# Optimization experiments

Hardware: AMD Instinct MI355X
Metric: run time of the kernel (lower is better)

## Reference

```python
import jax, jax.numpy as jnp
import numpy as np


def setup_inputs() -> dict:
    key = jax.random.key(0)
    ks = jax.random.split(key, 7)
    B, L, D, H = 256, 1024, 768, 768
    x = jax.random.normal(ks[0], (B, L, D), dtype=jnp.float32)
    label_mask = jax.random.randint(ks[1], (B, L), 0, 2).astype(jnp.int32)
    global_prototype_tensor = jax.random.normal(ks[2], (L + 1, D), dtype=jnp.float32)
    W_h = jax.random.normal(ks[3], (H, D), dtype=jnp.float32) * 0.02
    b_h = jax.random.normal(ks[4], (H,), dtype=jnp.float32) * 0.02
    W_p = jax.random.normal(ks[5], (D, H), dtype=jnp.float32) * 0.02
    b_p = jax.random.normal(ks[6], (D,), dtype=jnp.float32) * 0.02
    return {"x": x, "label_mask": label_mask,
            "global_prototype_tensor": global_prototype_tensor,
            "W_h": W_h, "b_h": b_h, "W_p": W_p, "b_p": b_p}


def _mlp(v, W_h, b_h, W_p, b_p):
    # torch Linear: y = v @ W.T + b
    h = jax.nn.relu(jnp.einsum('ld,hd->lh', v, W_h) + b_h)
    return jnp.einsum('lh,dh->ld', h, W_p) + b_p


def reference(x, label_mask, global_prototype_tensor, W_h, b_h, W_p, b_p):
    # x: [B, L, D]; label_mask: [B, L] (1 if label i in example's label_list)
    m = label_mask.astype(x.dtype)                        # [B, L]
    pos_cnt = m.sum(0)                                    # [L]
    B = x.shape[0]
    anti_cnt = B - pos_cnt                                # [L]
    pos_sum = jnp.einsum('bl,bld->ld', m, x)              # masked segment-sum
    tot_sum = x.sum(0)                                    # [L, D]
    anti_sum = tot_sum - pos_sum

    pos_mean = pos_sum / jnp.maximum(pos_cnt, 1.0)[:, None]
    anti_mean = anti_sum / jnp.maximum(anti_cnt, 1.0)[:, None]

    avg_pos = 0.5 * pos_mean + 0.5 * global_prototype_tensor[:-1]   # [L, D]
    avg_anti = 0.5 * anti_mean + 0.5 * global_prototype_tensor[-1]  # [L, D]

    proto = _mlp(avg_pos, W_h, b_h, W_p, b_p)
    proto = jnp.where((pos_cnt > 0)[:, None], proto, 0.0)           # rows stay zero if no members

    anti_proto = _mlp(avg_anti, W_h, b_h, W_p, b_p)
    w = (anti_cnt > 0).astype(x.dtype)                              # [L]
    anti = jnp.einsum('l,ld->d', w, anti_proto) / jnp.maximum(w.sum(), 1.0)

    return jnp.concatenate([proto, anti[None, :]], axis=0)          # [L+1, D]
```

## Files before the change

### kernel.cpp

```cpp
#include <hip/hip_runtime.h>

#define L_DIM 1024
#define B_DIM 256
#define D_DIM 768
#define K_DIM 768
#define NT    (K_DIM / 32)
#define WN    (768 * 768)

typedef _Float16 half8 __attribute__((ext_vector_type(8)));
typedef float    floatx4 __attribute__((ext_vector_type(4)));

__device__ __forceinline__ ushort f2h(float f) {
    _Float16 h = (_Float16)f;
    return __builtin_bit_cast(ushort, h);
}
__device__ __forceinline__ float h2f(ushort u) {
    return (float)__builtin_bit_cast(_Float16, u);
}

__device__ __forceinline__ void gl16(const ushort* g, ushort* l) {
    __builtin_amdgcn_global_load_lds(
        (const __attribute__((address_space(1))) unsigned int*)g,
        (__attribute__((address_space(3))) unsigned int*)l, 16, 0, 0);
}

__global__ __launch_bounds__(768)
void reduce_and_cast(const float* __restrict__ x,
                     const int* __restrict__ mask,
                     const float* __restrict__ gpt,
                     const float* __restrict__ Wh, const float* __restrict__ Wp,
                     ushort* __restrict__ Vhi, ushort* __restrict__ Vlo,
                     ushort* __restrict__ WhH, ushort* __restrict__ WpH,
                     float* __restrict__ pos_cnt)
{
    const int tid = threadIdx.x;

    if (blockIdx.x >= 256) {
        const int idx = ((blockIdx.x - 256) * 768 + tid) * 4;
        const float4 v = (idx < WN) ? *(const float4*)(Wh + idx)
                                    : *(const float4*)(Wp + (idx - WN));
        ushort4 o;
        o.x = f2h(v.x); o.y = f2h(v.y); o.z = f2h(v.z); o.w = f2h(v.w);
        if (idx < WN) *(ushort4*)(WhH + idx) = o;
        else          *(ushort4*)(WpH + (idx - WN)) = o;
        return;
    }

    __shared__ int mS[256][4];
    const int l0 = blockIdx.x * 4;
    if (tid < 256)
        *(int4*)&mS[tid][0] = *(const int4*)(mask + (size_t)tid * L_DIM + l0);
    __syncthreads();

    const int row = tid / 192;
    const int t   = tid % 192;
    const int d0  = t * 4;
    const int l   = l0 + row;

    const size_t bstride = (size_t)L_DIM * D_DIM;
    const float* xp = x + (size_t)l * D_DIM + d0;

    floatx4 pos = {0.f, 0.f, 0.f, 0.f};
    floatx4 tot = {0.f, 0.f, 0.f, 0.f};
    float cnt = 0.f;

    #pragma unroll 16
    for (int b = 0; b < B_DIM; ++b) {
        const floatx4 v = __builtin_nontemporal_load((const floatx4*)(xp + (size_t)b * bstride));
        const float fm = (float)mS[b][row];
        tot += v;
        pos[0] = fmaf(fm, v[0], pos[0]);
        pos[1] = fmaf(fm, v[1], pos[1]);
        pos[2] = fmaf(fm, v[2], pos[2]);
        pos[3] = fmaf(fm, v[3], pos[3]);
        cnt += fm;
    }

    const float inv_p = 0.5f / fmaxf(cnt, 1.0f);
    const float inv_a = 0.5f / fmaxf((float)B_DIM - cnt, 1.0f);

    const float4 g4  = *(const float4*)(gpt + (size_t)l * D_DIM + d0);
    const float4 gl4 = *(const float4*)(gpt + (size_t)L_DIM * D_DIM + d0);

    float vp[4], va[4];
    vp[0] = pos[0] * inv_p + 0.5f * g4.x;
    vp[1] = pos[1] * inv_p + 0.5f * g4.y;
    vp[2] = pos[2] * inv_p + 0.5f * g4.z;
    vp[3] = pos[3] * inv_p + 0.5f * g4.w;
    va[0] = (tot[0] - pos[0]) * inv_a + 0.5f * gl4.x;
    va[1] = (tot[1] - pos[1]) * inv_a + 0.5f * gl4.y;
    va[2] = (tot[2] - pos[2]) * inv_a + 0.5f * gl4.z;
    va[3] = (tot[3] - pos[3]) * inv_a + 0.5f * gl4.w;

    ushort4 ph, pl, ah, al;
    ph.x = f2h(vp[0]); pl.x = f2h(vp[0] - h2f(ph.x));
    ph.y = f2h(vp[1]); pl.y = f2h(vp[1] - h2f(ph.y));
    ph.z = f2h(vp[2]); pl.z = f2h(vp[2] - h2f(ph.z));
    ph.w = f2h(vp[3]); pl.w = f2h(vp[3] - h2f(ph.w));
    ah.x = f2h(va[0]); al.x = f2h(va[0] - h2f(ah.x));
    ah.y = f2h(va[1]); al.y = f2h(va[1] - h2f(ah.y));
    ah.z = f2h(va[2]); al.z = f2h(va[2] - h2f(ah.z));
    ah.w = f2h(va[3]); al.w = f2h(va[3] - h2f(ah.w));

    const size_t r0 = (size_t)l * D_DIM + d0;
    const size_t r1 = (size_t)(L_DIM + l) * D_DIM + d0;
    *(ushort4*)(Vhi + r0) = ph;  *(ushort4*)(Vlo + r0) = pl;
    *(ushort4*)(Vhi + r1) = ah;  *(ushort4*)(Vlo + r1) = al;

    if (t == 0) pos_cnt[l] = cnt;
}

template<int MODE>
__global__ __launch_bounds__(256)
void gemm_split(const ushort* __restrict__ Ahi, const ushort* __restrict__ Alo,
                const ushort* __restrict__ Bh, const float* __restrict__ bias,
                ushort* __restrict__ OutHi, ushort* __restrict__ OutLo,
                float* __restrict__ OutF, float* __restrict__ Partial,
                const float* __restrict__ cnt)
{
    __shared__ ushort lds[2][3][64 * 32];
    __shared__ float  colsum[4][32];

    const int tid  = threadIdx.x;
    const int lane = tid & 63;
    const int wid  = tid >> 6;
    const int brow = blockIdx.y * 64;
    const int bcol = blockIdx.x * 64;
    const int wr   = (wid >> 1) * 32;
    const int wc   = (wid & 1) * 32;

    const int srow = tid >> 2;
    const int slot = tid & 3;
    const int sk   = (slot ^ ((srow >> 1) & 3)) * 8;

    const ushort* pAh = Ahi + (size_t)(brow + srow) * K_DIM + sk;
    const ushort* pAl = Alo + (size_t)(brow + srow) * K_DIM + sk;
    const ushort* pBh = Bh  + (size_t)(bcol + srow) * K_DIM + sk;

    const int ldst = tid * 8;

    const int q   = lane >> 4;
    const int rA  = wr + (lane & 15);
    const int rB  = wc + (lane & 15);
    const int fA  = rA * 32 + ((q ^ ((rA >> 1) & 3)) << 3);
    const int fB  = rB * 32 + ((q ^ ((rB >> 1) & 3)) << 3);

    floatx4 acc[2][2] = {};

    gl16(pAh, &lds[0][0][ldst]);
    gl16(pAl, &lds[0][1][ldst]);
    gl16(pBh, &lds[0][2][ldst]);
    __syncthreads();

    for (int t = 0; t < NT; ++t) {
        const int cur = t & 1;
        if (t + 1 < NT) {
            const int ko = (t + 1) * 32;
            const int nxt = cur ^ 1;
            gl16(pAh + ko, &lds[nxt][0][ldst]);
            gl16(pAl + ko, &lds[nxt][1][ldst]);
            gl16(pBh + ko, &lds[nxt][2][ldst]);
        }
        half8 ah0 = *(half8*)&lds[cur][0][fA];
        half8 ah1 = *(half8*)&lds[cur][0][fA + 512];
        half8 al0 = *(half8*)&lds[cur][1][fA];
        half8 al1 = *(half8*)&lds[cur][1][fA + 512];
        half8 bh0 = *(half8*)&lds[cur][2][fB];
        half8 bh1 = *(half8*)&lds[cur][2][fB + 512];

        acc[0][0] = __builtin_amdgcn_mfma_f32_16x16x32_f16(ah0, bh0, acc[0][0], 0, 0, 0);
        acc[0][1] = __builtin_amdgcn_mfma_f32_16x16x32_f16(ah0, bh1, acc[0][1], 0, 0, 0);
        acc[1][0] = __builtin_amdgcn_mfma_f32_16x16x32_f16(ah1, bh0, acc[1][0], 0, 0, 0);
        acc[1][1] = __builtin_amdgcn_mfma_f32_16x16x32_f16(ah1, bh1, acc[1][1], 0, 0, 0);
        acc[0][0] = __builtin_amdgcn_mfma_f32_16x16x32_f16(al0, bh0, acc[0][0], 0, 0, 0);
        acc[0][1] = __builtin_amdgcn_mfma_f32_16x16x32_f16(al0, bh1, acc[0][1], 0, 0, 0);
        acc[1][0] = __builtin_amdgcn_mfma_f32_16x16x32_f16(al1, bh0, acc[1][0], 0, 0, 0);
        acc[1][1] = __builtin_amdgcn_mfma_f32_16x16x32_f16(al1, bh1, acc[1][1], 0, 0, 0);

        __syncthreads();
    }

    if (MODE == 0 || brow < L_DIM) {
        #pragma unroll
        for (int mi = 0; mi < 2; ++mi) {
            #pragma unroll
            for (int ni = 0; ni < 2; ++ni) {
                const int col   = bcol + wc + ni * 16 + (lane & 15);
                const int rbase = brow + wr + mi * 16 + ((lane >> 4) << 2);
                const float bv = bias[col];
                #pragma unroll
                for (int r = 0; r < 4; ++r) {
                    const float v = acc[mi][ni][r] + bv;
                    const int row = rbase + r;
                    if (MODE == 0) {
                        const float h = fmaxf(v, 0.f);
                        const ushort hh = f2h(h);
                        OutHi[(size_t)row * D_DIM + col] = hh;
                        OutLo[(size_t)row * D_DIM + col] = f2h(h - h2f(hh));
                    } else {
                        OutF[(size_t)row * D_DIM + col] = (cnt[row] > 0.f) ? v : 0.f;
                    }
                }
            }
        }
    } else {
        float s[2] = {0.f, 0.f};
        #pragma unroll
        for (int mi = 0; mi < 2; ++mi) {
            const int rbase = brow + wr + mi * 16 + ((lane >> 4) << 2);
            #pragma unroll
            for (int r = 0; r < 4; ++r) {
                const float w = (cnt[rbase + r - L_DIM] < 255.5f) ? 1.0f : 0.0f;
                #pragma unroll
                for (int ni = 0; ni < 2; ++ni) {
                    const int col = bcol + wc + ni * 16 + (lane & 15);
                    s[ni] = fmaf(w, acc[mi][ni][r] + bias[col], s[ni]);
                }
            }
        }
        #pragma unroll
        for (int ni = 0; ni < 2; ++ni) {
            s[ni] += __shfl_down(s[ni], 32);
            s[ni] += __shfl_down(s[ni], 16);
            if (lane < 16) colsum[wid][ni * 16 + lane] = s[ni];
        }
        __syncthreads();
        if (tid < 64) {
            const float v = (tid < 32)
                ? colsum[0][tid] + colsum[2][tid]
                : colsum[1][tid - 32] + colsum[3][tid - 32];
            Partial[(size_t)(blockIdx.y - 16) * D_DIM + bcol + tid] = v;
        }
    }
}

__global__ __launch_bounds__(256)
void finalize_anti(const float* __restrict__ Partial,
                   const float* __restrict__ cnt,
                   float* __restrict__ out)
{
    const int d = blockIdx.x * 256 + threadIdx.x;
    float s = 0.f;
    #pragma unroll
    for (int p = 0; p < 16; ++p) s += Partial[(size_t)p * D_DIM + d];
    float wsum = 0.f;
    #pragma unroll 8
    for (int l = 0; l < L_DIM; ++l) wsum += (cnt[l] < 255.5f) ? 1.0f : 0.0f;
    out[(size_t)L_DIM * D_DIM + d] = s / fmaxf(wsum, 1.0f);
}

extern "C" void kernel_launch(void* const* d_in, const int* in_sizes, int n_in,
                              void* d_out, int out_size, void* d_ws, size_t ws_size,
                              hipStream_t stream) {
    const float* x    = (const float*)d_in[0];
    const int*   mask = (const int*)d_in[1];
    const float* gpt  = (const float*)d_in[2];
    const float* W_h  = (const float*)d_in[3];
    const float* b_h  = (const float*)d_in[4];
    const float* W_p  = (const float*)d_in[5];
    const float* b_p  = (const float*)d_in[6];
    float* out = (float*)d_out;

    char* p = (char*)d_ws;
    ushort* Vhi  = (ushort*)p; p += (size_t)2 * L_DIM * D_DIM * 2;
    ushort* Vlo  = (ushort*)p; p += (size_t)2 * L_DIM * D_DIM * 2;
    ushort* Hhi  = (ushort*)p; p += (size_t)2 * L_DIM * D_DIM * 2;
    ushort* Hlo  = (ushort*)p; p += (size_t)2 * L_DIM * D_DIM * 2;
    ushort* WhH  = (ushort*)p; p += (size_t)WN * 2;
    ushort* WpH  = (ushort*)p; p += (size_t)WN * 2;
    float*  Part = (float*)p;  p += (size_t)16 * D_DIM * 4;
    float*  cnt  = (float*)p;

    reduce_and_cast<<<640, 768, 0, stream>>>(x, mask, gpt, W_h, W_p,
                                             Vhi, Vlo, WhH, WpH, cnt);

    dim3 ggrid(D_DIM / 64, 2 * L_DIM / 64);
    gemm_split<0><<<ggrid, 256, 0, stream>>>(Vhi, Vlo, WhH, b_h,
                                             Hhi, Hlo, nullptr, nullptr, nullptr);
    gemm_split<1><<<ggrid, 256, 0, stream>>>(Hhi, Hlo, WpH, b_p,
                                             nullptr, nullptr, out, Part, cnt);

    finalize_anti<<<3, 256, 0, stream>>>(Part, cnt, out);
}
```

Measured before the change: 187.0 us.

## Split batch reduction across two block halves with a separate combine kernel

The reduction over the batch now runs in twice as many smaller blocks: each block covers two labels and half of the batch, and writes partial pos/tot sums and counts to workspace. A new combine kernel adds the two partials, applies the mean and prototype blend, and emits the hi/lo half-precision split. The weight-cast blocks are reorganised to 384 threads and placed first in the grid. The aim is more parallelism and better occupancy on the bandwidth-bound read of x, at the cost of an extra kernel launch and a write and read of the partial buffers.

```diff
diff --git a/kernel.cpp b/kernel.cpp
--- a/kernel.cpp
+++ b/kernel.cpp
@@ -6,6 +6,8 @@
 #define K_DIM 768
 #define NT    (K_DIM / 32)
 #define WN    (768 * 768)
+#define CAST_BLOCKS 768
+#define RED_BLOCKS  1024
 
 typedef _Float16 half8 __attribute__((ext_vector_type(8)));
 typedef float    floatx4 __attribute__((ext_vector_type(4)));
@@ -24,19 +26,18 @@
         (__attribute__((address_space(3))) unsigned int*)l, 16, 0, 0);
 }
 
-__global__ __launch_bounds__(768)
+__global__ __launch_bounds__(384, 6)
 void reduce_and_cast(const float* __restrict__ x,
                      const int* __restrict__ mask,
-                     const float* __restrict__ gpt,
                      const float* __restrict__ Wh, const float* __restrict__ Wp,
-                     ushort* __restrict__ Vhi, ushort* __restrict__ Vlo,
-                     ushort* __restrict__ WhH, ushort* __restrict__ WpH,
-                     float* __restrict__ pos_cnt)
+                     float* __restrict__ posP, float* __restrict__ totP,
+                     float* __restrict__ cntP,
+                     ushort* __restrict__ WhH, ushort* __restrict__ WpH)
 {
     const int tid = threadIdx.x;
 
-    if (blockIdx.x >= 256) {
-        const int idx = ((blockIdx.x - 256) * 768 + tid) * 4;
+    if (blockIdx.x < CAST_BLOCKS) {
+        const int idx = (blockIdx.x * 384 + tid) * 4;
         const float4 v = (idx < WN) ? *(const float4*)(Wh + idx)
                                     : *(const float4*)(Wp + (idx - WN));
         ushort4 o;
@@ -46,10 +47,14 @@
         return;
     }
 
-    __shared__ int mS[256][4];
-    const int l0 = blockIdx.x * 4;
-    if (tid < 256)
-        *(int4*)&mS[tid][0] = *(const int4*)(mask + (size_t)tid * L_DIM + l0);
+    const int bi = blockIdx.x - CAST_BLOCKS;
+    const int lq = bi >> 1;
+    const int bh = bi & 1;
+    const int l0 = lq * 2;
+
+    __shared__ int mS[128][2];
+    if (tid < 128)
+        *(int2*)&mS[tid][0] = *(const int2*)(mask + (size_t)(bh * 128 + tid) * L_DIM + l0);
     __syncthreads();
 
     const int row = tid / 192;
@@ -58,14 +63,14 @@
     const int l   = l0 + row;
 
     const size_t bstride = (size_t)L_DIM * D_DIM;
-    const float* xp = x + (size_t)l * D_DIM + d0;
+    const float* xp = x + (size_t)(bh * 128) * bstride + (size_t)l * D_DIM + d0;
 
     floatx4 pos = {0.f, 0.f, 0.f, 0.f};
     floatx4 tot = {0.f, 0.f, 0.f, 0.f};
     float cnt = 0.f;
 
-    #pragma unroll 16
-    for (int b = 0; b < B_DIM; ++b) {
+    #pragma unroll 8
+    for (int b = 0; b < 128; ++b) {
         const floatx4 v = __builtin_nontemporal_load((const floatx4*)(xp + (size_t)b * bstride));
         const float fm = (float)mS[b][row];
         tot += v;
@@ -76,6 +81,32 @@
         cnt += fm;
     }
 
+    const size_t po = (size_t)(bh * L_DIM + l) * D_DIM + d0;
+    *(floatx4*)(posP + po) = pos;
+    *(floatx4*)(totP + po) = tot;
+    if (t == 0) cntP[bh * L_DIM + l] = cnt;
+}
+
+__global__ __launch_bounds__(192)
+void combine_build_v(const float* __restrict__ posP, const float* __restrict__ totP,
+                     const float* __restrict__ cntP,
+                     const float* __restrict__ gpt,
+                     ushort* __restrict__ Vhi, ushort* __restrict__ Vlo,
+                     float* __restrict__ pos_cnt)
+{
+    const int l  = blockIdx.x;
+    const int d0 = threadIdx.x * 4;
+    const size_t o0 = (size_t)l * D_DIM + d0;
+    const size_t o1 = (size_t)(L_DIM + l) * D_DIM + d0;
+
+    const floatx4 p0 = *(const floatx4*)(posP + o0);
+    const floatx4 p1 = *(const floatx4*)(posP + o1);
+    const floatx4 t0 = *(const floatx4*)(totP + o0);
+    const floatx4 t1 = *(const floatx4*)(totP + o1);
+    const floatx4 pos = p0 + p1;
+    const floatx4 tot = t0 + t1;
+    const float cnt = cntP[l] + cntP[L_DIM + l];
+
     const float inv_p = 0.5f / fmaxf(cnt, 1.0f);
     const float inv_a = 0.5f / fmaxf((float)B_DIM - cnt, 1.0f);
 
@@ -102,12 +133,10 @@
     ah.z = f2h(va[2]); al.z = f2h(va[2] - h2f(ah.z));
     ah.w = f2h(va[3]); al.w = f2h(va[3] - h2f(ah.w));
 
-    const size_t r0 = (size_t)l * D_DIM + d0;
-    const size_t r1 = (size_t)(L_DIM + l) * D_DIM + d0;
-    *(ushort4*)(Vhi + r0) = ph;  *(ushort4*)(Vlo + r0) = pl;
-    *(ushort4*)(Vhi + r1) = ah;  *(ushort4*)(Vlo + r1) = al;
-
-    if (t == 0) pos_cnt[l] = cnt;
+    *(ushort4*)(Vhi + o0) = ph;  *(ushort4*)(Vlo + o0) = pl;
+    *(ushort4*)(Vhi + o1) = ah;  *(ushort4*)(Vlo + o1) = al;
+
+    if (threadIdx.x == 0) pos_cnt[l] = cnt;
 }
 
 template<int MODE>
@@ -268,11 +297,16 @@
     ushort* Hlo  = (ushort*)p; p += (size_t)2 * L_DIM * D_DIM * 2;
     ushort* WhH  = (ushort*)p; p += (size_t)WN * 2;
     ushort* WpH  = (ushort*)p; p += (size_t)WN * 2;
+    float*  posP = (float*)p;  p += (size_t)2 * L_DIM * D_DIM * 4;
+    float*  totP = (float*)p;  p += (size_t)2 * L_DIM * D_DIM * 4;
+    float*  cntP = (float*)p;  p += (size_t)2 * L_DIM * 4;
     float*  Part = (float*)p;  p += (size_t)16 * D_DIM * 4;
     float*  cnt  = (float*)p;
 
-    reduce_and_cast<<<640, 768, 0, stream>>>(x, mask, gpt, W_h, W_p,
-                                             Vhi, Vlo, WhH, WpH, cnt);
+    reduce_and_cast<<<CAST_BLOCKS + RED_BLOCKS, 384, 0, stream>>>(
+        x, mask, W_h, W_p, posP, totP, cntP, WhH, WpH);
+
+    combine_build_v<<<L_DIM, 192, 0, stream>>>(posP, totP, cntP, gpt, Vhi, Vlo, cnt);
 
     dim3 ggrid(D_DIM / 64, 2 * L_DIM / 64);
     gemm_split<0><<<ggrid, 256, 0, stream>>>(Vhi, Vlo, WhH, b_h,
```

Measured after the change: 214.5 us. +14.7%, slower.

## Widen GEMM tiles to 64x128 and fold anti-finalize into last block

Applied to the files above, without the earlier changes.

The split-precision GEMM tile grows from 64x64 to 64x128 columns per block, so each wave computes 2x4 MFMA tiles and A-fragment loads are reused across more columns. The grid shrinks from 384 to 192 blocks. The separate finalize_anti launch is removed: the last block of the second GEMM, found with an atomic counter and threadfence, sums the partials and weights. This saves a launch and reduces A traffic, at the cost of fewer blocks (192 on a 256-CU part), which leaves compute units idle, plus a serial tail in the last block.

```diff
diff --git a/kernel.cpp b/kernel.cpp
--- a/kernel.cpp
+++ b/kernel.cpp
@@ -4,7 +4,7 @@
 #define B_DIM 256
 #define D_DIM 768
 #define K_DIM 768
-#define NT    (K_DIM / 32)
+#define NTILES (K_DIM / 32)
 #define WN    (768 * 768)
 
 typedef _Float16 half8 __attribute__((ext_vector_type(8)));
@@ -31,7 +31,7 @@
                      const float* __restrict__ Wh, const float* __restrict__ Wp,
                      ushort* __restrict__ Vhi, ushort* __restrict__ Vlo,
                      ushort* __restrict__ WhH, ushort* __restrict__ WpH,
-                     float* __restrict__ pos_cnt)
+                     float* __restrict__ pos_cnt, unsigned* __restrict__ counter)
 {
     const int tid = threadIdx.x;
 
@@ -45,6 +45,8 @@
         else          *(ushort4*)(WpH + (idx - WN)) = o;
         return;
     }
+
+    if (blockIdx.x == 0 && tid == 0) *counter = 0u;
 
     __shared__ int mS[256][4];
     const int l0 = blockIdx.x * 4;
@@ -116,18 +118,20 @@
                 const ushort* __restrict__ Bh, const float* __restrict__ bias,
                 ushort* __restrict__ OutHi, ushort* __restrict__ OutLo,
                 float* __restrict__ OutF, float* __restrict__ Partial,
-                const float* __restrict__ cnt)
+                const float* __restrict__ cnt, unsigned* __restrict__ counter)
 {
-    __shared__ ushort lds[2][3][64 * 32];
-    __shared__ float  colsum[4][32];
+    __shared__ ushort lds[2][8192];
+    __shared__ float  colsum[4][64];
+    __shared__ float  red[256];
+    __shared__ unsigned lastflag;
 
     const int tid  = threadIdx.x;
     const int lane = tid & 63;
     const int wid  = tid >> 6;
     const int brow = blockIdx.y * 64;
-    const int bcol = blockIdx.x * 64;
+    const int bcol = blockIdx.x * 128;
     const int wr   = (wid >> 1) * 32;
-    const int wc   = (wid & 1) * 32;
+    const int wc   = (wid & 1) * 64;
 
     const int srow = tid >> 2;
     const int slot = tid & 3;
@@ -135,47 +139,60 @@
 
     const ushort* pAh = Ahi + (size_t)(brow + srow) * K_DIM + sk;
     const ushort* pAl = Alo + (size_t)(brow + srow) * K_DIM + sk;
-    const ushort* pBh = Bh  + (size_t)(bcol + srow) * K_DIM + sk;
+    const ushort* pB0 = Bh  + (size_t)(bcol + srow) * K_DIM + sk;
+    const ushort* pB1 = Bh  + (size_t)(bcol + 64 + srow) * K_DIM + sk;
 
     const int ldst = tid * 8;
 
-    const int q   = lane >> 4;
-    const int rA  = wr + (lane & 15);
-    const int rB  = wc + (lane & 15);
-    const int fA  = rA * 32 + ((q ^ ((rA >> 1) & 3)) << 3);
-    const int fB  = rB * 32 + ((q ^ ((rB >> 1) & 3)) << 3);
-
-    floatx4 acc[2][2] = {};
-
-    gl16(pAh, &lds[0][0][ldst]);
-    gl16(pAl, &lds[0][1][ldst]);
-    gl16(pBh, &lds[0][2][ldst]);
+    const int q  = lane >> 4;
+    const int rA = wr + (lane & 15);
+    const int rB = wc + (lane & 15);
+    const int fA = rA * 32 + ((q ^ ((rA >> 1) & 3)) << 3);
+    const int fB = 4096 + rB * 32 + ((q ^ ((rB >> 1) & 3)) << 3);
+
+    floatx4 acc[2][4] = {};
+
+    gl16(pAh, &lds[0][ldst]);
+    gl16(pAl, &lds[0][2048 + ldst]);
+    gl16(pB0, &lds[0][4096 + ldst]);
+    gl16(pB1, &lds[0][6144 + ldst]);
     __syncthreads();
 
-    for (int t = 0; t < NT; ++t) {
+    for (int t = 0; t < NTILES; ++t) {
         const int cur = t & 1;
-        if (t + 1 < NT) {
+        if (t + 1 < NTILES) {
             const int ko = (t + 1) * 32;
             const int nxt = cur ^ 1;
-            gl16(pAh + ko, &lds[nxt][0][ldst]);
-            gl16(pAl + ko, &lds[nxt][1][ldst]);
-            gl16(pBh + ko, &lds[nxt][2][ldst]);
-        }
-        half8 ah0 = *(half8*)&lds[cur][0][fA];
-        half8 ah1 = *(half8*)&lds[cur][0][fA + 512];
-        half8 al0 = *(half8*)&lds[cur][1][fA];
-        half8 al1 = *(half8*)&lds[cur][1][fA + 512];
-        half8 bh0 = *(half8*)&lds[cur][2][fB];
-        half8 bh1 = *(half8*)&lds[cur][2][fB + 512];
-
-        acc[0][0] = __builtin_amdgcn_mfma_f32_16x16x32_f16(ah0, bh0, acc[0][0], 0, 0, 0);
-        acc[0][1] = __builtin_amdgcn_mfma_f32_16x16x32_f16(ah0, bh1, acc[0][1], 0, 0, 0);
-        acc[1][0] = __builtin_amdgcn_mfma_f32_16x16x32_f16(ah1, bh0, acc[1][0], 0, 0, 0);
-        acc[1][1] = __builtin_amdgcn_mfma_f32_16x16x32_f16(ah1, bh1, acc[1][1], 0, 0, 0);
-        acc[0][0] = __builtin_amdgcn_mfma_f32_16x16x32_f16(al0, bh0, acc[0][0], 0, 0, 0);
-        acc[0][1] = __builtin_amdgcn_mfma_f32_16x16x32_f16(al0, bh1, acc[0][1], 0, 0, 0);
-        acc[1][0] = __builtin_amdgcn_mfma_f32_16x16x32_f16(al1, bh0, acc[1][0], 0, 0, 0);
-        acc[1][1] = __builtin_amdgcn_mfma_f32_16x16x32_f16(al1, bh1, acc[1][1], 0, 0, 0);
+            gl16(pAh + ko, &lds[nxt][ldst]);
+            gl16(pAl + ko, &lds[nxt][2048 + ldst]);
+            gl16(pB0 + ko, &lds[nxt][4096 + ldst]);
+            gl16(pB1 + ko, &lds[nxt][6144 + ldst]);
+        }
+        half8 ah0 = *(half8*)&lds[cur][fA];
+        half8 ah1 = *(half8*)&lds[cur][fA + 512];
+        half8 al0 = *(half8*)&lds[cur][2048 + fA];
+        half8 al1 = *(half8*)&lds[cur][2048 + fA + 512];
+        half8 b0  = *(half8*)&lds[cur][fB];
+        half8 b1  = *(half8*)&lds[cur][fB + 512];
+        half8 b2  = *(half8*)&lds[cur][fB + 1024];
+        half8 b3  = *(half8*)&lds[cur][fB + 1536];
+
+        acc[0][0] = __builtin_amdgcn_mfma_f32_16x16x32_f16(ah0, b0, acc[0][0], 0, 0, 0);
+        acc[0][1] = __builtin_amdgcn_mfma_f32_16x16x32_f16(ah0, b1, acc[0][1], 0, 0, 0);
+        acc[0][2] = __builtin_amdgcn_mfma_f32_16x16x32_f16(ah0, b2, acc[0][2], 0, 0, 0);
+        acc[0][3] = __builtin_amdgcn_mfma_f32_16x16x32_f16(ah0, b3, acc[0][3], 0, 0, 0);
+        acc[1][0] = __builtin_amdgcn_mfma_f32_16x16x32_f16(ah1, b0, acc[1][0], 0, 0, 0);
+        acc[1][1] = __builtin_amdgcn_mfma_f32_16x16x32_f16(ah1, b1, acc[1][1], 0, 0, 0);
+        acc[1][2] = __builtin_amdgcn_mfma_f32_16x16x32_f16(ah1, b2, acc[1][2], 0, 0, 0);
+        acc[1][3] = __builtin_amdgcn_mfma_f32_16x16x32_f16(ah1, b3, acc[1][3], 0, 0, 0);
+        acc[0][0] = __builtin_amdgcn_mfma_f32_16x16x32_f16(al0, b0, acc[0][0], 0, 0, 0);
+        acc[0][1] = __builtin_amdgcn_mfma_f32_16x16x32_f16(al0, b1, acc[0][1], 0, 0, 0);
+        acc[0][2] = __builtin_amdgcn_mfma_f32_16x16x32_f16(al0, b2, acc[0][2], 0, 0, 0);
+        acc[0][3] = __builtin_amdgcn_mfma_f32_16x16x32_f16(al0, b3, acc[0][3], 0, 0, 0);
+        acc[1][0] = __builtin_amdgcn_mfma_f32_16x16x32_f16(al1, b0, acc[1][0], 0, 0, 0);
+        acc[1][1] = __builtin_amdgcn_mfma_f32_16x16x32_f16(al1, b1, acc[1][1], 0, 0, 0);
+        acc[1][2] = __builtin_amdgcn_mfma_f32_16x16x32_f16(al1, b2, acc[1][2], 0, 0, 0);
+        acc[1][3] = __builtin_amdgcn_mfma_f32_16x16x32_f16(al1, b3, acc[1][3], 0, 0, 0);
 
         __syncthreads();
     }
@@ -184,9 +201,9 @@
         #pragma unroll
         for (int mi = 0; mi < 2; ++mi) {
             #pragma unroll
-            for (int ni = 0; ni < 2; ++ni) {
+            for (int ni = 0; ni < 4; ++ni) {
                 const int col   = bcol + wc + ni * 16 + (lane & 15);
-                const int rbase = brow + wr + mi * 16 + ((lane >> 4) << 2);
+                const int rbase = brow + wr + mi * 16 + (q << 2);
                 const float bv = bias[col];
                 #pragma unroll
                 for (int r = 0; r < 4; ++r) {
@@ -204,49 +221,60 @@
             }
         }
     } else {
-        float s[2] = {0.f, 0.f};
+        float s[4] = {0.f, 0.f, 0.f, 0.f};
         #pragma unroll
         for (int mi = 0; mi < 2; ++mi) {
-            const int rbase = brow + wr + mi * 16 + ((lane >> 4) << 2);
+            const int rbase = brow + wr + mi * 16 + (q << 2);
             #pragma unroll
             for (int r = 0; r < 4; ++r) {
                 const float w = (cnt[rbase + r - L_DIM] < 255.5f) ? 1.0f : 0.0f;
                 #pragma unroll
-                for (int ni = 0; ni < 2; ++ni) {
+                for (int ni = 0; ni < 4; ++ni) {
                     const int col = bcol + wc + ni * 16 + (lane & 15);
                     s[ni] = fmaf(w, acc[mi][ni][r] + bias[col], s[ni]);
                 }
             }
         }
         #pragma unroll
-        for (int ni = 0; ni < 2; ++ni) {
+        for (int ni = 0; ni < 4; ++ni) {
             s[ni] += __shfl_down(s[ni], 32);
             s[ni] += __shfl_down(s[ni], 16);
             if (lane < 16) colsum[wid][ni * 16 + lane] = s[ni];
         }
         __syncthreads();
-        if (tid < 64) {
-            const float v = (tid < 32)
+        if (tid < 128) {
+            const float v = (tid < 64)
                 ? colsum[0][tid] + colsum[2][tid]
-                : colsum[1][tid - 32] + colsum[3][tid - 32];
+                : colsum[1][tid - 64] + colsum[3][tid - 64];
             Partial[(size_t)(blockIdx.y - 16) * D_DIM + bcol + tid] = v;
         }
+        __threadfence();
+        __syncthreads();
+        if (tid == 0) lastflag = (atomicAdd(counter, 1u) == 95u) ? 1u : 0u;
+        __syncthreads();
+        if (lastflag) {
+            __threadfence();
+            float w = 0.f;
+            for (int i = tid; i < L_DIM; i += 256)
+                w += (cnt[i] < 255.5f) ? 1.0f : 0.0f;
+            red[tid] = w;
+            __syncthreads();
+            for (int st = 128; st > 0; st >>= 1) {
+                if (tid < st) red[tid] += red[tid + st];
+                __syncthreads();
+            }
+            const float wsum = fmaxf(red[0], 1.0f);
+            #pragma unroll
+            for (int j = 0; j < 3; ++j) {
+                const int d = tid + j * 256;
+                float sm = 0.f;
+                #pragma unroll
+                for (int pp = 0; pp < 16; ++pp)
+                    sm += Partial[(size_t)pp * D_DIM + d];
+                OutF[(size_t)L_DIM * D_DIM + d] = sm / wsum;
+            }
+        }
     }
-}
-
-__global__ __launch_bounds__(256)
-void finalize_anti(const float* __restrict__ Partial,
-                   const float* __restrict__ cnt,
-                   float* __restrict__ out)
-{
-    const int d = blockIdx.x * 256 + threadIdx.x;
-    float s = 0.f;
-    #pragma unroll
-    for (int p = 0; p < 16; ++p) s += Partial[(size_t)p * D_DIM + d];
-    float wsum = 0.f;
-    #pragma unroll 8
-    for (int l = 0; l < L_DIM; ++l) wsum += (cnt[l] < 255.5f) ? 1.0f : 0.0f;
-    out[(size_t)L_DIM * D_DIM + d] = s / fmaxf(wsum, 1.0f);
 }
 
 extern "C" void kernel_launch(void* const* d_in, const int* in_sizes, int n_in,
@@ -269,16 +297,15 @@
     ushort* WhH  = (ushort*)p; p += (size_t)WN * 2;
     ushort* WpH  = (ushort*)p; p += (size_t)WN * 2;
     float*  Part = (float*)p;  p += (size_t)16 * D_DIM * 4;
-    float*  cnt  = (float*)p;
+    float*  cnt  = (float*)p;  p += (size_t)L_DIM * 4;
+    unsigned* counter = (unsigned*)p;
 
     reduce_and_cast<<<640, 768, 0, stream>>>(x, mask, gpt, W_h, W_p,
-                                             Vhi, Vlo, WhH, WpH, cnt);
-
-    dim3 ggrid(D_DIM / 64, 2 * L_DIM / 64);
+                                             Vhi, Vlo, WhH, WpH, cnt, counter);
+
+    dim3 ggrid(D_DIM / 128, 2 * L_DIM / 64);
     gemm_split<0><<<ggrid, 256, 0, stream>>>(Vhi, Vlo, WhH, b_h,
-                                             Hhi, Hlo, nullptr, nullptr, nullptr);
+                                             Hhi, Hlo, nullptr, nullptr, nullptr, nullptr);
     gemm_split<1><<<ggrid, 256, 0, stream>>>(Hhi, Hlo, WpH, b_p,
-                                             nullptr, nullptr, out, Part, cnt);
-
-    finalize_anti<<<3, 256, 0, stream>>>(Part, cnt, out);
-}
+                                             nullptr, nullptr, out, Part, cnt, counter);
+}
```

Result: no change. 184.4 us (-1.4%).
